# Performance work log

Measured on AMD Instinct MI355X. Metric: run time of the kernel, lower is better.

Reference implementation:

```python
import jax, jax.numpy as jnp
import numpy as np

B, N, X, H = 128, 512, 128, 256  # batch, seq len, in features, hidden

_PARAM_SHAPES = [
    ("fg_w_c", (H,)), ("fg_w_h", (H, H)), ("fg_w_x", (H, X)), ("fg_b", (H,)),
    ("ig_w_c", (H,)), ("ig_w_h", (H, H)), ("ig_w_x", (H, X)), ("ig_b", (H,)),
    ("in_w_h", (H, H)), ("in_w_x", (H, X)), ("in_b", (H,)),
    ("og_w_cn", (H,)), ("og_w_h", (H, H)), ("og_w_x", (H, X)), ("og_b", (H,)), ("og_w_t", (H,)),
    ("tg1_w_x", (H, X)), ("tg1_w_t", (H,)), ("tg1_b", (H,)),
    ("tg2_w_x", (H, X)), ("tg2_w_t", (H,)), ("tg2_b", (H,)),
]


def setup_inputs() -> dict:
    key = jax.random.key(0)
    ks = jax.random.split(key, 2 + len(_PARAM_SHAPES))
    stdv = 1.0 / np.sqrt(H)  # torch __init__ re-inits all params uniform(-stdv, stdv)
    inp = {
        "x": jax.random.normal(ks[0], (B, N, X), jnp.float32),
        "t": jax.random.uniform(ks[1], (B, N, 1), jnp.float32),  # time intervals >= 0
    }
    for i, (name, shape) in enumerate(_PARAM_SHAPES):
        inp[name] = jax.random.uniform(ks[2 + i], shape, jnp.float32, -stdv, stdv)
    return inp


def reference(x, t,
              fg_w_c, fg_w_h, fg_w_x, fg_b,
              ig_w_c, ig_w_h, ig_w_x, ig_b,
              in_w_h, in_w_x, in_b,
              og_w_cn, og_w_h, og_w_x, og_b, og_w_t,
              tg1_w_x, tg1_w_t, tg1_b,
              tg2_w_x, tg2_w_t, tg2_b):
    # TimeLSTM_v3 with nn_type = NN_TYPE_LSTM_TIME2.
    # torch stores vector params as [H,1] and x_cur as [B,xm,1]; here squeezed to [H] / [B,xm].
    # Precompute all input-dependent (non-recurrent) gate terms over the whole sequence: [B,N,H]
    fg_x = jnp.einsum('bnx,hx->bnh', x, fg_w_x) + fg_b
    ig_x = jnp.einsum('bnx,hx->bnh', x, ig_w_x) + ig_b
    in_x = jnp.einsum('bnx,hx->bnh', x, in_w_x) + in_b
    og_x = jnp.einsum('bnx,hx->bnh', x, og_w_x) + og_w_t * t + og_b
    # Time gates depend only on x and t -> fully precomputable
    tm1 = jax.nn.sigmoid(jnp.einsum('bnx,hx->bnh', x, tg1_w_x) + jnp.tanh(tg1_w_t * t) + tg1_b)
    tm2 = jax.nn.sigmoid(jnp.einsum('bnx,hx->bnh', x, tg2_w_x) + jnp.tanh(tg2_w_t * t) + tg2_b)

    def step(carry, inputs):
        h, cm = carry  # each [B,H]
        fg_xt, ig_xt, in_xt, og_xt, tm1_t, tm2_t = inputs
        ig = jax.nn.sigmoid(ig_w_c * cm + h @ ig_w_h.T + ig_xt)
        fg = jax.nn.sigmoid(fg_w_c * cm + h @ fg_w_h.T + fg_xt)
        inn = jnp.tanh(h @ in_w_h.T + in_xt)
        cm_hat = fg * cm + ig * tm1_t * inn
        cm_new = fg * cm + ig * tm2_t * inn
        og = jax.nn.sigmoid(og_w_cn * cm_hat + h @ og_w_h.T + og_xt)
        h_new = og * jnp.tanh(cm_hat)
        return (h_new, cm_new), None

    seqs = tuple(jnp.moveaxis(a, 1, 0) for a in (fg_x, ig_x, in_x, og_x, tm1, tm2))  # [N,B,H]
    init = (jnp.zeros((x.shape[0], H), x.dtype), jnp.zeros((x.shape[0], H), x.dtype))
    (h, cm), _ = jax.lax.scan(step, init, seqs)
    return h, cm  # h: [B,H] (torch squeezes trailing 1), cm: [B,H]
```

## Files before the change

kernel.cpp:

```cpp
#include <hip/hip_runtime.h>
#include <math.h>

#define BATCH 128
#define SEQN  512
#define XF    128
#define HF    256
#define BC    16
#define HC    8
#define TCH   8
#define NBLK  256
#define NTHR  256
#define NGRP  8
#define GSZ   32

#define OFF_W    0
#define OFF_WX   8192
#define OFF_G    14336
#define OFF_X    20480
#define OFF_CM   36864
#define OFF_TV   36992
#define OFF_COEF 37120
#define OFF_GO   37216
#define LDS_WORDS 37220
#define LDS_BYTES (LDS_WORDS * 4)

struct Params {
  const float* x;
  const float* t;
  const float* w_h[4];
  const float* w_x[6];
  const float* coef[12];
  float* h_buf;
  unsigned* flags;
  float* out;
};

__device__ __forceinline__ float sigmoidf_(float v) { return 1.0f / (1.0f + __expf(-v)); }

__device__ __forceinline__ float swzx1(float v) { return __int_as_float(__builtin_amdgcn_ds_swizzle(__float_as_int(v), 0x041F)); }
__device__ __forceinline__ float swzx2(float v) { return __int_as_float(__builtin_amdgcn_ds_swizzle(__float_as_int(v), 0x081F)); }
__device__ __forceinline__ float swzx4(float v) { return __int_as_float(__builtin_amdgcn_ds_swizzle(__float_as_int(v), 0x101F)); }

__device__ __forceinline__ void post_arrive(unsigned* flags, int gi, int mi, unsigned step) {
  __syncthreads();
  if (threadIdx.x == 0) {
    __hip_atomic_store(&flags[(gi * GSZ + mi) * 16], step,
                       __ATOMIC_RELAXED, __HIP_MEMORY_SCOPE_AGENT);
  }
}

__device__ __forceinline__ void wave_wait(float* sm, const unsigned* flags,
                                          int gi, int mi, unsigned step) {
  unsigned* go = (unsigned*)&sm[OFF_GO];
  const int tid = threadIdx.x;
  if (tid < 64) {
    const bool need = (tid < GSZ) && (tid != mi);
    const unsigned* f = &flags[(gi * GSZ + (tid & (GSZ - 1))) * 16];
    while (true) {
      unsigned v = need ? __hip_atomic_load(f, __ATOMIC_RELAXED, __HIP_MEMORY_SCOPE_AGENT)
                        : step;
      if (__all((int)(v >= step))) break;
    }
    if (tid == 0)
      __hip_atomic_store(go, step, __ATOMIC_RELAXED, __HIP_MEMORY_SCOPE_WORKGROUP);
  } else {
    while (__hip_atomic_load(go, __ATOMIC_RELAXED, __HIP_MEMORY_SCOPE_WORKGROUP) < step) {}
  }
}

__global__ __launch_bounds__(NTHR, 1) void timelstm_kernel(Params p) {
  extern __shared__ float sm[];
  const int tid = threadIdx.x;
  const int bid = blockIdx.x;
  const int gi = bid & 7;
  const int mi = bid >> 3;
  const int b0 = gi * BC;
  const int h0 = mi * HC;

  for (int i = tid; i < 4 * 8 * 256; i += NTHR) {
    int g = i >> 11, j = (i >> 8) & 7, k = i & 255;
    sm[OFF_W + k * 32 + j * 4 + g] = p.w_h[g][(h0 + j) * HF + k];
  }
  for (int i = tid; i < 6 * 8 * 128; i += NTHR) {
    int g = i >> 10, j = (i >> 7) & 7, k = i & 127;
    sm[OFF_WX + k * 48 + j * 6 + g] = p.w_x[g][(h0 + j) * XF + k];
  }
  if (tid < 96) sm[OFF_COEF + tid] = p.coef[tid >> 3][h0 + (tid & 7)];
  if (tid < 128) sm[OFF_CM + tid] = 0.0f;
  if (tid == 0) *(unsigned*)&sm[OFF_GO] = 0u;
  if (mi == 0) {
    unsigned long long* hbu = (unsigned long long*)p.h_buf;
    for (int i = tid; i < HF * BC / 2; i += NTHR) {
      const int k = i >> 3;
      __hip_atomic_store(&hbu[k * (BATCH / 2) + b0 / 2 + (i & 7)], 0ull,
                         __ATOMIC_RELAXED, __HIP_MEMORY_SCOPE_AGENT);
    }
  }
  post_arrive(p.flags, gi, mi, 1u);
  unsigned bstep = 1;
  int cur = 0;

  const int lane = tid & 63;
  const int bq = tid >> 6;
  const int kh = lane & 7;
  const int j  = lane >> 3;

  for (int tc0 = 0; tc0 < SEQN; tc0 += TCH) {
    {
      float4 xr[16];
#pragma unroll
      for (int it = 0; it < 16; ++it) {
        const int ri = it * 8 + (tid >> 5);
        const int k0 = (tid & 31) * 4;
        xr[it] = *(const float4*)&p.x[((size_t)(b0 + (ri >> 3)) * SEQN + (tc0 + (ri & 7))) * XF + k0];
      }
#pragma unroll
      for (int it = 0; it < 16; ++it) {
        const int ri = it * 8 + (tid >> 5);
        const int k0 = (tid & 31) * 4;
        const float xb[4] = {xr[it].x, xr[it].y, xr[it].z, xr[it].w};
#pragma unroll
        for (int u = 0; u < 4; ++u) {
          const int k = k0 + u;
          sm[OFF_X + k * 128 + (ri ^ (((k >> 2) & 7) << 2))] = xb[u];
        }
      }
      if (tid < 128)
        sm[OFF_TV + tid] = p.t[(size_t)(b0 + (tid >> 3)) * SEQN + tc0 + (tid & 7)];
    }
    __syncthreads();
    {
      const int c = tid >> 3, r = tid & 7;
      const int c4 = c << 2;
      float a0[4], a1[4], a2[4], a3[4], a4[4], a5[4];
#pragma unroll
      for (int u = 0; u < 4; ++u) { a0[u]=0.f; a1[u]=0.f; a2[u]=0.f; a3[u]=0.f; a4[u]=0.f; a5[u]=0.f; }
      const float* wxp = &sm[OFF_WX + r * 6];
#pragma unroll 4
      for (int k = 0; k < XF; ++k) {
        const float4 xv = *(const float4*)&sm[OFF_X + k * 128 + (c4 ^ (((k >> 2) & 7) << 2))];
        const float2 wA = *(const float2*)&wxp[k * 48 + 0];
        const float2 wB = *(const float2*)&wxp[k * 48 + 2];
        const float2 wC = *(const float2*)&wxp[k * 48 + 4];
        const float xs[4] = {xv.x, xv.y, xv.z, xv.w};
#pragma unroll
        for (int u = 0; u < 4; ++u) {
          a0[u] += wA.x * xs[u]; a1[u] += wA.y * xs[u];
          a2[u] += wB.x * xs[u]; a3[u] += wB.y * xs[u];
          a4[u] += wC.x * xs[u]; a5[u] += wC.y * xs[u];
        }
      }
      const float cfg  = sm[OFF_COEF + 0 * 8 + r], cig  = sm[OFF_COEF + 1 * 8 + r];
      const float cin  = sm[OFF_COEF + 2 * 8 + r];
      const float cogb = sm[OFF_COEF + 3 * 8 + r], cogwt = sm[OFF_COEF + 4 * 8 + r];
      const float ct1w = sm[OFF_COEF + 5 * 8 + r], ct1b = sm[OFF_COEF + 6 * 8 + r];
      const float ct2w = sm[OFF_COEF + 7 * 8 + r], ct2b = sm[OFF_COEF + 8 * 8 + r];
#pragma unroll
      for (int u = 0; u < 4; ++u) {
        const int bt = c4 + u, b = bt >> 3, t = bt & 7;
        const float tv = sm[OFF_TV + bt];
        float* gp = &sm[OFF_G + t * 768 + b * 8 + r];
        gp[0]   = a0[u] + cfg;
        gp[128] = a1[u] + cig;
        gp[256] = a2[u] + cin;
        gp[384] = a3[u] + cogwt * tv + cogb;
        gp[512] = sigmoidf_(a4[u] + tanhf(ct1w * tv) + ct1b);
        gp[640] = sigmoidf_(a5[u] + tanhf(ct2w * tv) + ct2b);
      }
    }
    __syncthreads();

    for (int tt = 0; tt < TCH; ++tt) {
      wave_wait(sm, p.flags, gi, mi, bstep);
      {
        const unsigned long long* hsrc =
            (const unsigned long long*)(p.h_buf + (size_t)cur * HF * BATCH);
        unsigned long long uv[8];
#pragma unroll
        for (int it = 0; it < 8; ++it) {
          const int i = it * 256 + tid;
          const int k = i >> 3;
          uv[it] = __hip_atomic_load(&hsrc[k * (BATCH / 2) + b0 / 2 + (i & 7)],
                                     __ATOMIC_RELAXED, __HIP_MEMORY_SCOPE_AGENT);
        }
#pragma unroll
        for (int it = 0; it < 8; ++it) {
          const int i = it * 256 + tid;
          const int k = i >> 3, pr = i & 7;
          union { unsigned long long u; float2 f; } cv;
          cv.u = uv[it];
          *(float2*)&sm[OFF_X + k * 16 + ((pr * 2) ^ (((k >> 5) & 3) << 2))] = cv.f;
        }
      }
      __syncthreads();

      float acc[4][4];
#pragma unroll
      for (int bi = 0; bi < 4; ++bi)
#pragma unroll
        for (int g = 0; g < 4; ++g) acc[bi][g] = 0.f;

      const float* hp = &sm[OFF_X + kh * 512 + ((bq ^ (kh & 3)) << 2)];
      const float* wp = &sm[OFF_W + kh * 1024 + (j << 2)];
#pragma unroll 8
      for (int kk = 0; kk < 32; ++kk) {
        const float4 hv = *(const float4*)&hp[kk * 16];
        const float4 wv = *(const float4*)&wp[kk * 32];
        acc[0][0] += hv.x * wv.x; acc[0][1] += hv.x * wv.y; acc[0][2] += hv.x * wv.z; acc[0][3] += hv.x * wv.w;
        acc[1][0] += hv.y * wv.x; acc[1][1] += hv.y * wv.y; acc[1][2] += hv.y * wv.z; acc[1][3] += hv.y * wv.w;
        acc[2][0] += hv.z * wv.x; acc[2][1] += hv.z * wv.y; acc[2][2] += hv.z * wv.z; acc[2][3] += hv.z * wv.w;
        acc[3][0] += hv.w * wv.x; acc[3][1] += hv.w * wv.y; acc[3][2] += hv.w * wv.z; acc[3][3] += hv.w * wv.w;
      }

      const int kb0 = kh & 1, kb1 = (kh >> 1) & 1;
      float s1[2][4];
#pragma unroll
      for (int pp = 0; pp < 2; ++pp)
#pragma unroll
        for (int g = 0; g < 4; ++g) {
          const float mine  = kb0 ? acc[2 * pp + 1][g] : acc[2 * pp][g];
          const float yours = kb0 ? acc[2 * pp][g]     : acc[2 * pp + 1][g];
          s1[pp][g] = mine + swzx1(yours);
        }
      float s2[4];
#pragma unroll
      for (int g = 0; g < 4; ++g) {
        const float mine  = kb1 ? s1[1][g] : s1[0][g];
        const float yours = kb1 ? s1[0][g] : s1[1][g];
        s2[g] = mine + swzx2(yours);
      }
      float pre[4];
#pragma unroll
      for (int g = 0; g < 4; ++g) pre[g] = s2[g] + swzx4(s2[g]);

      {
        const int bi = kh & 3;
        const int b  = (bq << 2) + bi;
        const int ib = b * 8 + j;
        const float cm = sm[OFF_CM + ib];
        const float* gt = &sm[OFF_G + tt * 768 + ib];
        const float fgx = gt[0],   igx = gt[128], inx = gt[256];
        const float ogx = gt[384], tm1 = gt[512], tm2 = gt[640];
        const float igv = sigmoidf_(sm[OFF_COEF + 10 * 8 + j] * cm + pre[1] + igx);
        const float fgv = sigmoidf_(sm[OFF_COEF + 9 * 8 + j] * cm + pre[0] + fgx);
        const float inn = tanhf(pre[2] + inx);
        const float cbase = fgv * cm, cinn = igv * inn;
        const float cmh = cbase + cinn * tm1;
        const float cmn = cbase + cinn * tm2;
        const float ogv = sigmoidf_(sm[OFF_COEF + 11 * 8 + j] * cmh + pre[3] + ogx);
        const float hn  = ogv * tanhf(cmh);
        const float hn2 = swzx1(hn);
        if (kh < 4) {
          sm[OFF_CM + ib] = cmn;
          if (!(kh & 1)) {
            union { float2 f; unsigned long long u; } cv;
            cv.f.x = hn; cv.f.y = hn2;
            unsigned long long* hdst =
                (unsigned long long*)(p.h_buf + (size_t)(cur ^ 1) * HF * BATCH +
                                      (size_t)(h0 + j) * BATCH + b0 + b);
            __hip_atomic_store(hdst, cv.u, __ATOMIC_RELAXED, __HIP_MEMORY_SCOPE_AGENT);
          }
          if (tc0 + tt == SEQN - 1) {
            p.out[(size_t)(b0 + b) * HF + h0 + j] = hn;
            p.out[(size_t)BATCH * HF + (size_t)(b0 + b) * HF + h0 + j] = cmn;
          }
        }
      }
      post_arrive(p.flags, gi, mi, bstep + 1);
      ++bstep;
      cur ^= 1;
    }
  }
}

extern "C" void kernel_launch(void* const* d_in, const int* in_sizes, int n_in,
                              void* d_out, int out_size, void* d_ws, size_t ws_size,
                              hipStream_t stream) {
  (void)in_sizes; (void)n_in; (void)out_size; (void)ws_size;
  Params p;
  p.x = (const float*)d_in[0];
  p.t = (const float*)d_in[1];
  p.w_h[0] = (const float*)d_in[3];
  p.w_h[1] = (const float*)d_in[7];
  p.w_h[2] = (const float*)d_in[10];
  p.w_h[3] = (const float*)d_in[14];
  p.w_x[0] = (const float*)d_in[4];
  p.w_x[1] = (const float*)d_in[8];
  p.w_x[2] = (const float*)d_in[11];
  p.w_x[3] = (const float*)d_in[15];
  p.w_x[4] = (const float*)d_in[18];
  p.w_x[5] = (const float*)d_in[21];
  p.coef[0]  = (const float*)d_in[5];
  p.coef[1]  = (const float*)d_in[9];
  p.coef[2]  = (const float*)d_in[12];
  p.coef[3]  = (const float*)d_in[16];
  p.coef[4]  = (const float*)d_in[17];
  p.coef[5]  = (const float*)d_in[19];
  p.coef[6]  = (const float*)d_in[20];
  p.coef[7]  = (const float*)d_in[22];
  p.coef[8]  = (const float*)d_in[23];
  p.coef[9]  = (const float*)d_in[2];
  p.coef[10] = (const float*)d_in[6];
  p.coef[11] = (const float*)d_in[13];
  p.flags = (unsigned*)d_ws;
  p.h_buf = (float*)((char*)d_ws + 32768);
  p.out = (float*)d_out;

  hipMemsetAsync(d_ws, 0, 16384, stream);
  hipFuncSetAttribute((const void*)timelstm_kernel,
                      hipFuncAttributeMaxDynamicSharedMemorySize, LDS_BYTES);
  timelstm_kernel<<<dim3(NBLK), dim3(NTHR), LDS_BYTES, stream>>>(p);
}
```

Baseline: 2.727 ms.

## Keep recurrent weights in registers and replace per-block flags with per-wave atomic counters

```diff
diff --git a/kernel.cpp b/kernel.cpp
--- a/kernel.cpp
+++ b/kernel.cpp
@@ -13,15 +13,13 @@
 #define NGRP  8
 #define GSZ   32
 
-#define OFF_W    0
-#define OFF_WX   8192
-#define OFF_G    14336
-#define OFF_X    20480
-#define OFF_CM   36864
-#define OFF_TV   36992
-#define OFF_COEF 37120
-#define OFF_GO   37216
-#define LDS_WORDS 37220
+#define OFF_WX   0
+#define OFF_G    6144
+#define OFF_X    12288
+#define OFF_CM   28672
+#define OFF_TV   28800
+#define OFF_COEF 28928
+#define LDS_WORDS 29024
 #define LDS_BYTES (LDS_WORDS * 4)
 
 struct Params {
@@ -31,7 +29,7 @@
   const float* w_x[6];
   const float* coef[12];
   float* h_buf;
-  unsigned* flags;
+  unsigned* ctr;
   float* out;
 };
 
@@ -41,30 +39,23 @@
 __device__ __forceinline__ float swzx2(float v) { return __int_as_float(__builtin_amdgcn_ds_swizzle(__float_as_int(v), 0x081F)); }
 __device__ __forceinline__ float swzx4(float v) { return __int_as_float(__builtin_amdgcn_ds_swizzle(__float_as_int(v), 0x101F)); }
 
-__device__ __forceinline__ void post_arrive(unsigned* flags, int gi, int mi, unsigned step) {
-  __syncthreads();
-  if (threadIdx.x == 0) {
-    __hip_atomic_store(&flags[(gi * GSZ + mi) * 16], step,
-                       __ATOMIC_RELAXED, __HIP_MEMORY_SCOPE_AGENT);
+__device__ __forceinline__ void post_wave(unsigned* ctr, int gi) {
+  asm volatile("s_waitcnt vmcnt(0)" ::: "memory");
+  if ((threadIdx.x & 63) == 0) {
+    const int wv = threadIdx.x >> 6;
+    __hip_atomic_fetch_add(&ctr[(gi * 4 + wv) * 16], 1u,
+                           __ATOMIC_RELAXED, __HIP_MEMORY_SCOPE_AGENT);
   }
 }
 
-__device__ __forceinline__ void wave_wait(float* sm, const unsigned* flags,
-                                          int gi, int mi, unsigned step) {
-  unsigned* go = (unsigned*)&sm[OFF_GO];
-  const int tid = threadIdx.x;
-  if (tid < 64) {
-    const bool need = (tid < GSZ) && (tid != mi);
-    const unsigned* f = &flags[(gi * GSZ + (tid & (GSZ - 1))) * 16];
-    while (true) {
-      unsigned v = need ? __hip_atomic_load(f, __ATOMIC_RELAXED, __HIP_MEMORY_SCOPE_AGENT)
-                        : step;
-      if (__all((int)(v >= step))) break;
-    }
-    if (tid == 0)
-      __hip_atomic_store(go, step, __ATOMIC_RELAXED, __HIP_MEMORY_SCOPE_WORKGROUP);
-  } else {
-    while (__hip_atomic_load(go, __ATOMIC_RELAXED, __HIP_MEMORY_SCOPE_WORKGROUP) < step) {}
+__device__ __forceinline__ void wait_group(const unsigned* ctr, int gi, unsigned target) {
+  const int lane = threadIdx.x & 63;
+  const bool need = lane < 4;
+  const unsigned* f = &ctr[(gi * 4 + (lane & 3)) * 16];
+  while (true) {
+    unsigned v = need ? __hip_atomic_load(f, __ATOMIC_RELAXED, __HIP_MEMORY_SCOPE_AGENT)
+                      : 0u;
+    if (__all((int)(!need || v >= target))) break;
   }
 }
 
@@ -77,17 +68,26 @@
   const int b0 = gi * BC;
   const int h0 = mi * HC;
 
-  for (int i = tid; i < 4 * 8 * 256; i += NTHR) {
-    int g = i >> 11, j = (i >> 8) & 7, k = i & 255;
-    sm[OFF_W + k * 32 + j * 4 + g] = p.w_h[g][(h0 + j) * HF + k];
-  }
+  const int lane = tid & 63;
+  const int bq = tid >> 6;
+  const int kh = lane & 7;
+  const int j  = lane >> 3;
+
+  float wrs[4][32];
+#pragma unroll
+  for (int g = 0; g < 4; ++g)
+#pragma unroll
+    for (int q = 0; q < 8; ++q) {
+      const float4 v = *(const float4*)&p.w_h[g][(size_t)(h0 + j) * HF + kh * 32 + q * 4];
+      wrs[g][q * 4 + 0] = v.x; wrs[g][q * 4 + 1] = v.y;
+      wrs[g][q * 4 + 2] = v.z; wrs[g][q * 4 + 3] = v.w;
+    }
   for (int i = tid; i < 6 * 8 * 128; i += NTHR) {
-    int g = i >> 10, j = (i >> 7) & 7, k = i & 127;
-    sm[OFF_WX + k * 48 + j * 6 + g] = p.w_x[g][(h0 + j) * XF + k];
+    int g = i >> 10, jj = (i >> 7) & 7, k = i & 127;
+    sm[OFF_WX + k * 48 + jj * 6 + g] = p.w_x[g][(h0 + jj) * XF + k];
   }
   if (tid < 96) sm[OFF_COEF + tid] = p.coef[tid >> 3][h0 + (tid & 7)];
   if (tid < 128) sm[OFF_CM + tid] = 0.0f;
-  if (tid == 0) *(unsigned*)&sm[OFF_GO] = 0u;
   if (mi == 0) {
     unsigned long long* hbu = (unsigned long long*)p.h_buf;
     for (int i = tid; i < HF * BC / 2; i += NTHR) {
@@ -96,33 +96,31 @@
                          __ATOMIC_RELAXED, __HIP_MEMORY_SCOPE_AGENT);
     }
   }
-  post_arrive(p.flags, gi, mi, 1u);
-  unsigned bstep = 1;
+  post_wave(p.ctr, gi);
+  unsigned tstep = 1;
   int cur = 0;
 
-  const int lane = tid & 63;
-  const int bq = tid >> 6;
-  const int kh = lane & 7;
-  const int j  = lane >> 3;
-
   for (int tc0 = 0; tc0 < SEQN; tc0 += TCH) {
+    __syncthreads();
     {
-      float4 xr[16];
-#pragma unroll
-      for (int it = 0; it < 16; ++it) {
-        const int ri = it * 8 + (tid >> 5);
-        const int k0 = (tid & 31) * 4;
-        xr[it] = *(const float4*)&p.x[((size_t)(b0 + (ri >> 3)) * SEQN + (tc0 + (ri & 7))) * XF + k0];
-      }
-#pragma unroll
-      for (int it = 0; it < 16; ++it) {
-        const int ri = it * 8 + (tid >> 5);
-        const int k0 = (tid & 31) * 4;
-        const float xb[4] = {xr[it].x, xr[it].y, xr[it].z, xr[it].w};
-#pragma unroll
-        for (int u = 0; u < 4; ++u) {
-          const int k = k0 + u;
-          sm[OFF_X + k * 128 + (ri ^ (((k >> 2) & 7) << 2))] = xb[u];
+#pragma unroll
+      for (int half = 0; half < 2; ++half) {
+        float4 xr[8];
+#pragma unroll
+        for (int it = 0; it < 8; ++it) {
+          const int ri = (half * 8 + it) * 8 + (tid >> 5);
+          xr[it] = *(const float4*)&p.x[((size_t)(b0 + (ri >> 3)) * SEQN + (tc0 + (ri & 7))) * XF + (tid & 31) * 4];
+        }
+#pragma unroll
+        for (int it = 0; it < 8; ++it) {
+          const int ri = (half * 8 + it) * 8 + (tid >> 5);
+          const int k0 = (tid & 31) * 4;
+          const float xb[4] = {xr[it].x, xr[it].y, xr[it].z, xr[it].w};
+#pragma unroll
+          for (int u = 0; u < 4; ++u) {
+            const int k = k0 + u;
+            sm[OFF_X + k * 128 + (ri ^ (((k >> 2) & 7) << 2))] = xb[u];
+          }
         }
       }
       if (tid < 128)
@@ -171,7 +169,7 @@
     __syncthreads();
 
     for (int tt = 0; tt < TCH; ++tt) {
-      wave_wait(sm, p.flags, gi, mi, bstep);
+      wait_group(p.ctr, gi, 32u * tstep);
       {
         const unsigned long long* hsrc =
             (const unsigned long long*)(p.h_buf + (size_t)cur * HF * BATCH);
@@ -201,15 +199,14 @@
         for (int g = 0; g < 4; ++g) acc[bi][g] = 0.f;
 
       const float* hp = &sm[OFF_X + kh * 512 + ((bq ^ (kh & 3)) << 2)];
-      const float* wp = &sm[OFF_W + kh * 1024 + (j << 2)];
-#pragma unroll 8
+#pragma unroll
       for (int kk = 0; kk < 32; ++kk) {
         const float4 hv = *(const float4*)&hp[kk * 16];
-        const float4 wv = *(const float4*)&wp[kk * 32];
-        acc[0][0] += hv.x * wv.x; acc[0][1] += hv.x * wv.y; acc[0][2] += hv.x * wv.z; acc[0][3] += hv.x * wv.w;
-        acc[1][0] += hv.y * wv.x; acc[1][1] += hv.y * wv.y; acc[1][2] += hv.y * wv.z; acc[1][3] += hv.y * wv.w;
-        acc[2][0] += hv.z * wv.x; acc[2][1] += hv.z * wv.y; acc[2][2] += hv.z * wv.z; acc[2][3] += hv.z * wv.w;
-        acc[3][0] += hv.w * wv.x; acc[3][1] += hv.w * wv.y; acc[3][2] += hv.w * wv.z; acc[3][3] += hv.w * wv.w;
+        const float w0 = wrs[0][kk], w1 = wrs[1][kk], w2 = wrs[2][kk], w3 = wrs[3][kk];
+        acc[0][0] += hv.x * w0; acc[0][1] += hv.x * w1; acc[0][2] += hv.x * w2; acc[0][3] += hv.x * w3;
+        acc[1][0] += hv.y * w0; acc[1][1] += hv.y * w1; acc[1][2] += hv.y * w2; acc[1][3] += hv.y * w3;
+        acc[2][0] += hv.z * w0; acc[2][1] += hv.z * w1; acc[2][2] += hv.z * w2; acc[2][3] += hv.z * w3;
+        acc[3][0] += hv.w * w0; acc[3][1] += hv.w * w1; acc[3][2] += hv.w * w2; acc[3][3] += hv.w * w3;
       }
 
       const int kb0 = kh & 1, kb1 = (kh >> 1) & 1;
@@ -266,8 +263,8 @@
           }
         }
       }
-      post_arrive(p.flags, gi, mi, bstep + 1);
-      ++bstep;
+      post_wave(p.ctr, gi);
+      ++tstep;
       cur ^= 1;
     }
   }
@@ -302,7 +299,7 @@
   p.coef[9]  = (const float*)d_in[2];
   p.coef[10] = (const float*)d_in[6];
   p.coef[11] = (const float*)d_in[13];
-  p.flags = (unsigned*)d_ws;
+  p.ctr = (unsigned*)d_ws;
   p.h_buf = (float*)((char*)d_ws + 32768);
   p.out = (float*)d_out;
 
```

Result: slower. 5.557 ms (+103.8%).
